# Performance work log

Hardware: AMD Instinct MI355X
Metric: run time of the kernel (lower is better)

The kernel has to match this reference:

```python
import jax, jax.numpy as jnp
import numpy as np

EPS = 1e-5

def setup_inputs() -> dict:
    key = jax.random.key(0)
    k1, k2 = jax.random.split(key)
    N, C, B = 2000000, 32, 16
    data = jax.random.normal(k1, (N, C), dtype=jnp.float32)
    batch_id = jnp.sort(jax.random.randint(k2, (N,), 0, B, dtype=jnp.int32))
    weights = jnp.ones((1, C), dtype=jnp.float32)
    bias = jnp.zeros((1, C), dtype=jnp.float32)
    return {"data": data, "batch_id": batch_id, "batch_size": B,
            "weights": weights, "bias": bias}

def reference(data, batch_id, batch_size, weights, bias):
    # Per-octree (segment) instance norm over nodes, per channel.
    # count[b] = number of nodes in octree b
    ones = jnp.ones((data.shape[0], 1), dtype=data.dtype)
    count = jax.ops.segment_sum(ones, batch_id, num_segments=batch_size)  # [B,1]
    norm = 1.0 / (count + EPS)                                            # [B,1]
    mean = jax.ops.segment_sum(data, batch_id, num_segments=batch_size) * norm  # [B,C]
    out = data - mean[batch_id]                                           # [N,C]
    var = jax.ops.segment_sum(out * out, batch_id, num_segments=batch_size) * norm
    inv_std = 1.0 / jnp.sqrt(var + EPS)                                   # [B,C]
    out = out * inv_std[batch_id]
    return out * weights + bias
```

## Files before the change

kernel.cpp:

```cpp
#include <hip/hip_runtime.h>

#define EPS 1e-5f
#define NB 16
#define NC 32

__global__ __launch_bounds__(256) void oin_stats(
    const float* __restrict__ data,
    const int* __restrict__ batch_id,
    int N, int chunk,
    float* __restrict__ g_sum,
    float* __restrict__ g_sumsq,
    float* __restrict__ g_cnt)
{
    __shared__ float s_sum[NB * NC];
    __shared__ float s_sumsq[NB * NC];
    __shared__ float s_cnt[NB];

    for (int i = threadIdx.x; i < NB * NC; i += 256) { s_sum[i] = 0.f; s_sumsq[i] = 0.f; }
    if (threadIdx.x < NB) s_cnt[threadIdx.x] = 0.f;
    __syncthreads();

    const int c4    = threadIdx.x & 7;
    const int rlane = threadIdx.x >> 3;

    int start = blockIdx.x * chunk;
    int end   = start + chunk;
    if (end > N) end = N;

    const float4* __restrict__ d4 = (const float4*)data;

    float4 a  = make_float4(0.f, 0.f, 0.f, 0.f);
    float4 a2 = make_float4(0.f, 0.f, 0.f, 0.f);
    float  cnt = 0.f;
    int    cur = -1;

    for (int row = start + rlane; row < end; row += 32) {
        int b = batch_id[row];
        if (b != cur) {
            if (cur >= 0) {
                int base = cur * NC + c4 * 4;
                atomicAdd(&s_sum[base + 0], a.x);  atomicAdd(&s_sum[base + 1], a.y);
                atomicAdd(&s_sum[base + 2], a.z);  atomicAdd(&s_sum[base + 3], a.w);
                atomicAdd(&s_sumsq[base + 0], a2.x); atomicAdd(&s_sumsq[base + 1], a2.y);
                atomicAdd(&s_sumsq[base + 2], a2.z); atomicAdd(&s_sumsq[base + 3], a2.w);
                if (c4 == 0) atomicAdd(&s_cnt[cur], cnt);
            }
            cur = b;
            a  = make_float4(0.f, 0.f, 0.f, 0.f);
            a2 = make_float4(0.f, 0.f, 0.f, 0.f);
            cnt = 0.f;
        }
        float4 v = d4[row * 8 + c4];
        a.x  += v.x;       a.y  += v.y;       a.z  += v.z;       a.w  += v.w;
        a2.x += v.x * v.x; a2.y += v.y * v.y; a2.z += v.z * v.z; a2.w += v.w * v.w;
        cnt += 1.f;
    }
    if (cur >= 0) {
        int base = cur * NC + c4 * 4;
        atomicAdd(&s_sum[base + 0], a.x);  atomicAdd(&s_sum[base + 1], a.y);
        atomicAdd(&s_sum[base + 2], a.z);  atomicAdd(&s_sum[base + 3], a.w);
        atomicAdd(&s_sumsq[base + 0], a2.x); atomicAdd(&s_sumsq[base + 1], a2.y);
        atomicAdd(&s_sumsq[base + 2], a2.z); atomicAdd(&s_sumsq[base + 3], a2.w);
        if (c4 == 0) atomicAdd(&s_cnt[cur], cnt);
    }
    __syncthreads();

    for (int i = threadIdx.x; i < NB * NC; i += 256) {
        atomicAdd(&g_sum[i], s_sum[i]);
        atomicAdd(&g_sumsq[i], s_sumsq[i]);
    }
    if (threadIdx.x < NB) atomicAdd(&g_cnt[threadIdx.x], s_cnt[threadIdx.x]);
}

__global__ __launch_bounds__(512) void oin_finalize(
    const float* __restrict__ g_sum, const float* __restrict__ g_sumsq,
    const float* __restrict__ g_cnt,
    const float* __restrict__ weights, const float* __restrict__ bias,
    float* __restrict__ g_scale, float* __restrict__ g_shift)
{
    int tid = threadIdx.x;
    int b = tid >> 5, c = tid & 31;
    float count = g_cnt[b];
    float norm  = 1.f / (count + EPS);
    float mean  = g_sum[tid] * norm;
    float cn    = count * norm;
    float var   = g_sumsq[tid] * norm - (2.f - cn) * mean * mean;
    float inv_std = 1.f / sqrtf(var + EPS);
    float scale = inv_std * weights[c];
    g_scale[tid] = scale;
    g_shift[tid] = bias[c] - mean * scale;
}

__global__ __launch_bounds__(256) void oin_norm(
    const float* __restrict__ data,
    const int* __restrict__ batch_id,
    const float* __restrict__ g_scale,
    const float* __restrict__ g_shift,
    float* __restrict__ out, int n4)
{
    __shared__ float4 s_scale4[NB * NC / 4];
    __shared__ float4 s_shift4[NB * NC / 4];
    {
        float* ss = (float*)s_scale4;
        float* sh = (float*)s_shift4;
        for (int i = threadIdx.x; i < NB * NC; i += 256) {
            ss[i] = g_scale[i];
            sh[i] = g_shift[i];
        }
    }
    __syncthreads();

    const float4* __restrict__ in4 = (const float4*)data;
    float4* __restrict__ out4 = (float4*)out;

    int stride = gridDim.x * 256;
    for (int i = blockIdx.x * 256 + threadIdx.x; i < n4; i += stride) {
        int row = i >> 3;
        int c4  = i & 7;
        int b   = batch_id[row];
        float4 v = in4[i];
        float4 sc = s_scale4[b * 8 + c4];
        float4 sh = s_shift4[b * 8 + c4];
        float4 o;
        o.x = v.x * sc.x + sh.x;
        o.y = v.y * sc.y + sh.y;
        o.z = v.z * sc.z + sh.z;
        o.w = v.w * sc.w + sh.w;
        out4[i] = o;
    }
}

extern "C" void kernel_launch(void* const* d_in, const int* in_sizes, int n_in,
                              void* d_out, int out_size, void* d_ws, size_t ws_size,
                              hipStream_t stream) {
    const float* data     = (const float*)d_in[0];
    const int*   batch_id = (const int*)d_in[1];
    const float* weights  = (const float*)d_in[3];
    const float* bias     = (const float*)d_in[4];
    float* out = (float*)d_out;

    int N = in_sizes[0] / NC;

    float* g_sum   = (float*)d_ws;
    float* g_sumsq = g_sum + NB * NC;
    float* g_cnt   = g_sumsq + NB * NC;
    float* g_scale = g_cnt + NB;
    float* g_shift = g_scale + NB * NC;

    hipMemsetAsync(d_ws, 0, (size_t)(NB * NC * 2 + NB) * sizeof(float), stream);

    const int blocks1 = 1024;
    int chunk = (N + blocks1 - 1) / blocks1;
    oin_stats<<<blocks1, 256, 0, stream>>>(data, batch_id, N, chunk, g_sum, g_sumsq, g_cnt);

    oin_finalize<<<1, 512, 0, stream>>>(g_sum, g_sumsq, g_cnt, weights, bias, g_scale, g_shift);

    int n4 = N * (NC / 4);
    oin_norm<<<2048, 256, 0, stream>>>(data, batch_id, g_scale, g_shift, out, n4);
}
```

Baseline: 526.5 us.

## Add uniform-segment fast paths and fuse finalize into normalize kernel

Stats and normalize kernels now check whether a block's row chunk lies in a single segment. If so, they skip per-row batch_id lookups and use 4-way unrolled float4 loads to expose more memory parallelism. The finalize kernel is removed, and each normalize block recomputes scale/shift from the global sums in shared memory, saving a launch. Global atomics with zero partials are skipped. The cost is a redundant per-block finalize computation and extra code paths.

```diff
diff --git a/kernel.cpp b/kernel.cpp
--- a/kernel.cpp
+++ b/kernel.cpp
@@ -27,16 +27,67 @@
     int end   = start + chunk;
     if (end > N) end = N;
 
-    const float4* __restrict__ d4 = (const float4*)data;
-
-    float4 a  = make_float4(0.f, 0.f, 0.f, 0.f);
-    float4 a2 = make_float4(0.f, 0.f, 0.f, 0.f);
-    float  cnt = 0.f;
-    int    cur = -1;
-
-    for (int row = start + rlane; row < end; row += 32) {
-        int b = batch_id[row];
-        if (b != cur) {
+    if (start < N) {
+        const float4* __restrict__ d4 = (const float4*)data;
+        float4 a  = make_float4(0.f, 0.f, 0.f, 0.f);
+        float4 a2 = make_float4(0.f, 0.f, 0.f, 0.f);
+        float  cnt = 0.f;
+
+        int b0 = batch_id[start];
+        int b1 = batch_id[end - 1];
+
+        if (b0 == b1) {
+            int row = start + rlane;
+            for (; row + 96 < end; row += 128) {
+                float4 v0 = d4[row * 8 + c4];
+                float4 v1 = d4[(row + 32) * 8 + c4];
+                float4 v2 = d4[(row + 64) * 8 + c4];
+                float4 v3 = d4[(row + 96) * 8 + c4];
+                a.x += v0.x; a.y += v0.y; a.z += v0.z; a.w += v0.w;
+                a2.x += v0.x*v0.x; a2.y += v0.y*v0.y; a2.z += v0.z*v0.z; a2.w += v0.w*v0.w;
+                a.x += v1.x; a.y += v1.y; a.z += v1.z; a.w += v1.w;
+                a2.x += v1.x*v1.x; a2.y += v1.y*v1.y; a2.z += v1.z*v1.z; a2.w += v1.w*v1.w;
+                a.x += v2.x; a.y += v2.y; a.z += v2.z; a.w += v2.w;
+                a2.x += v2.x*v2.x; a2.y += v2.y*v2.y; a2.z += v2.z*v2.z; a2.w += v2.w*v2.w;
+                a.x += v3.x; a.y += v3.y; a.z += v3.z; a.w += v3.w;
+                a2.x += v3.x*v3.x; a2.y += v3.y*v3.y; a2.z += v3.z*v3.z; a2.w += v3.w*v3.w;
+                cnt += 4.f;
+            }
+            for (; row < end; row += 32) {
+                float4 v = d4[row * 8 + c4];
+                a.x += v.x; a.y += v.y; a.z += v.z; a.w += v.w;
+                a2.x += v.x*v.x; a2.y += v.y*v.y; a2.z += v.z*v.z; a2.w += v.w*v.w;
+                cnt += 1.f;
+            }
+            int base = b0 * NC + c4 * 4;
+            atomicAdd(&s_sum[base + 0], a.x);  atomicAdd(&s_sum[base + 1], a.y);
+            atomicAdd(&s_sum[base + 2], a.z);  atomicAdd(&s_sum[base + 3], a.w);
+            atomicAdd(&s_sumsq[base + 0], a2.x); atomicAdd(&s_sumsq[base + 1], a2.y);
+            atomicAdd(&s_sumsq[base + 2], a2.z); atomicAdd(&s_sumsq[base + 3], a2.w);
+            if (c4 == 0) atomicAdd(&s_cnt[b0], cnt);
+        } else {
+            int cur = -1;
+            for (int row = start + rlane; row < end; row += 32) {
+                float4 v = d4[row * 8 + c4];
+                int b = batch_id[row];
+                if (b != cur) {
+                    if (cur >= 0) {
+                        int base = cur * NC + c4 * 4;
+                        atomicAdd(&s_sum[base + 0], a.x);  atomicAdd(&s_sum[base + 1], a.y);
+                        atomicAdd(&s_sum[base + 2], a.z);  atomicAdd(&s_sum[base + 3], a.w);
+                        atomicAdd(&s_sumsq[base + 0], a2.x); atomicAdd(&s_sumsq[base + 1], a2.y);
+                        atomicAdd(&s_sumsq[base + 2], a2.z); atomicAdd(&s_sumsq[base + 3], a2.w);
+                        if (c4 == 0) atomicAdd(&s_cnt[cur], cnt);
+                    }
+                    cur = b;
+                    a  = make_float4(0.f, 0.f, 0.f, 0.f);
+                    a2 = make_float4(0.f, 0.f, 0.f, 0.f);
+                    cnt = 0.f;
+                }
+                a.x += v.x; a.y += v.y; a.z += v.z; a.w += v.w;
+                a2.x += v.x*v.x; a2.y += v.y*v.y; a2.z += v.z*v.z; a2.w += v.w*v.w;
+                cnt += 1.f;
+            }
             if (cur >= 0) {
                 int base = cur * NC + c4 * 4;
                 atomicAdd(&s_sum[base + 0], a.x);  atomicAdd(&s_sum[base + 1], a.y);
@@ -45,88 +96,102 @@
                 atomicAdd(&s_sumsq[base + 2], a2.z); atomicAdd(&s_sumsq[base + 3], a2.w);
                 if (c4 == 0) atomicAdd(&s_cnt[cur], cnt);
             }
-            cur = b;
-            a  = make_float4(0.f, 0.f, 0.f, 0.f);
-            a2 = make_float4(0.f, 0.f, 0.f, 0.f);
-            cnt = 0.f;
-        }
-        float4 v = d4[row * 8 + c4];
-        a.x  += v.x;       a.y  += v.y;       a.z  += v.z;       a.w  += v.w;
-        a2.x += v.x * v.x; a2.y += v.y * v.y; a2.z += v.z * v.z; a2.w += v.w * v.w;
-        cnt += 1.f;
-    }
-    if (cur >= 0) {
-        int base = cur * NC + c4 * 4;
-        atomicAdd(&s_sum[base + 0], a.x);  atomicAdd(&s_sum[base + 1], a.y);
-        atomicAdd(&s_sum[base + 2], a.z);  atomicAdd(&s_sum[base + 3], a.w);
-        atomicAdd(&s_sumsq[base + 0], a2.x); atomicAdd(&s_sumsq[base + 1], a2.y);
-        atomicAdd(&s_sumsq[base + 2], a2.z); atomicAdd(&s_sumsq[base + 3], a2.w);
-        if (c4 == 0) atomicAdd(&s_cnt[cur], cnt);
+        }
     }
     __syncthreads();
 
     for (int i = threadIdx.x; i < NB * NC; i += 256) {
-        atomicAdd(&g_sum[i], s_sum[i]);
-        atomicAdd(&g_sumsq[i], s_sumsq[i]);
-    }
-    if (threadIdx.x < NB) atomicAdd(&g_cnt[threadIdx.x], s_cnt[threadIdx.x]);
-}
-
-__global__ __launch_bounds__(512) void oin_finalize(
-    const float* __restrict__ g_sum, const float* __restrict__ g_sumsq,
-    const float* __restrict__ g_cnt,
-    const float* __restrict__ weights, const float* __restrict__ bias,
-    float* __restrict__ g_scale, float* __restrict__ g_shift)
-{
-    int tid = threadIdx.x;
-    int b = tid >> 5, c = tid & 31;
-    float count = g_cnt[b];
-    float norm  = 1.f / (count + EPS);
-    float mean  = g_sum[tid] * norm;
-    float cn    = count * norm;
-    float var   = g_sumsq[tid] * norm - (2.f - cn) * mean * mean;
-    float inv_std = 1.f / sqrtf(var + EPS);
-    float scale = inv_std * weights[c];
-    g_scale[tid] = scale;
-    g_shift[tid] = bias[c] - mean * scale;
+        float s = s_sum[i], q = s_sumsq[i];
+        if (s != 0.f || q != 0.f) {
+            atomicAdd(&g_sum[i], s);
+            atomicAdd(&g_sumsq[i], q);
+        }
+    }
+    if (threadIdx.x < NB) {
+        float c = s_cnt[threadIdx.x];
+        if (c != 0.f) atomicAdd(&g_cnt[threadIdx.x], c);
+    }
 }
 
 __global__ __launch_bounds__(256) void oin_norm(
     const float* __restrict__ data,
     const int* __restrict__ batch_id,
-    const float* __restrict__ g_scale,
-    const float* __restrict__ g_shift,
-    float* __restrict__ out, int n4)
+    const float* __restrict__ g_sum,
+    const float* __restrict__ g_sumsq,
+    const float* __restrict__ g_cnt,
+    const float* __restrict__ weights,
+    const float* __restrict__ bias,
+    float* __restrict__ out, int N, int chunk)
 {
-    __shared__ float4 s_scale4[NB * NC / 4];
-    __shared__ float4 s_shift4[NB * NC / 4];
+    __shared__ float4 s_sc[NB * NC / 4];
+    __shared__ float4 s_sh[NB * NC / 4];
     {
-        float* ss = (float*)s_scale4;
-        float* sh = (float*)s_shift4;
-        for (int i = threadIdx.x; i < NB * NC; i += 256) {
-            ss[i] = g_scale[i];
-            sh[i] = g_shift[i];
+        float* sc = (float*)s_sc;
+        float* sh = (float*)s_sh;
+        for (int t = threadIdx.x; t < NB * NC; t += 256) {
+            int b = t >> 5, c = t & 31;
+            float count = g_cnt[b];
+            float norm  = 1.f / (count + EPS);
+            float mean  = g_sum[t] * norm;
+            float cn    = count * norm;
+            float var   = g_sumsq[t] * norm - (2.f - cn) * mean * mean;
+            float inv_std = 1.f / sqrtf(var + EPS);
+            float scale = inv_std * weights[c];
+            sc[t] = scale;
+            sh[t] = bias[c] - mean * scale;
         }
     }
     __syncthreads();
+
+    int start = blockIdx.x * chunk;
+    int end   = start + chunk;
+    if (end > N) end = N;
+    if (start >= N) return;
 
     const float4* __restrict__ in4 = (const float4*)data;
     float4* __restrict__ out4 = (float4*)out;
 
-    int stride = gridDim.x * 256;
-    for (int i = blockIdx.x * 256 + threadIdx.x; i < n4; i += stride) {
-        int row = i >> 3;
-        int c4  = i & 7;
-        int b   = batch_id[row];
-        float4 v = in4[i];
-        float4 sc = s_scale4[b * 8 + c4];
-        float4 sh = s_shift4[b * 8 + c4];
-        float4 o;
-        o.x = v.x * sc.x + sh.x;
-        o.y = v.y * sc.y + sh.y;
-        o.z = v.z * sc.z + sh.z;
-        o.w = v.w * sc.w + sh.w;
-        out4[i] = o;
+    int e0 = start * 8;
+    int e1 = end * 8;
+
+    int b0 = batch_id[start];
+    int b1 = batch_id[end - 1];
+
+    if (b0 == b1) {
+        float4 sc = s_sc[b0 * 8 + (threadIdx.x & 7)];
+        float4 sh = s_sh[b0 * 8 + (threadIdx.x & 7)];
+        int i = e0 + threadIdx.x;
+        for (; i + 768 < e1; i += 1024) {
+            float4 v0 = in4[i];
+            float4 v1 = in4[i + 256];
+            float4 v2 = in4[i + 512];
+            float4 v3 = in4[i + 768];
+            float4 o0, o1, o2, o3;
+            o0.x = v0.x*sc.x + sh.x; o0.y = v0.y*sc.y + sh.y; o0.z = v0.z*sc.z + sh.z; o0.w = v0.w*sc.w + sh.w;
+            o1.x = v1.x*sc.x + sh.x; o1.y = v1.y*sc.y + sh.y; o1.z = v1.z*sc.z + sh.z; o1.w = v1.w*sc.w + sh.w;
+            o2.x = v2.x*sc.x + sh.x; o2.y = v2.y*sc.y + sh.y; o2.z = v2.z*sc.z + sh.z; o2.w = v2.w*sc.w + sh.w;
+            o3.x = v3.x*sc.x + sh.x; o3.y = v3.y*sc.y + sh.y; o3.z = v3.z*sc.z + sh.z; o3.w = v3.w*sc.w + sh.w;
+            out4[i]       = o0;
+            out4[i + 256] = o1;
+            out4[i + 512] = o2;
+            out4[i + 768] = o3;
+        }
+        for (; i < e1; i += 256) {
+            float4 v = in4[i];
+            float4 o;
+            o.x = v.x*sc.x + sh.x; o.y = v.y*sc.y + sh.y; o.z = v.z*sc.z + sh.z; o.w = v.w*sc.w + sh.w;
+            out4[i] = o;
+        }
+    } else {
+        for (int i = e0 + threadIdx.x; i < e1; i += 256) {
+            float4 v = in4[i];
+            int b = batch_id[i >> 3];
+            float4 sc = s_sc[b * 8 + (i & 7)];
+            float4 sh = s_sh[b * 8 + (i & 7)];
+            float4 o;
+            o.x = v.x*sc.x + sh.x; o.y = v.y*sc.y + sh.y; o.z = v.z*sc.z + sh.z; o.w = v.w*sc.w + sh.w;
+            out4[i] = o;
+        }
     }
 }
 
@@ -144,17 +209,15 @@
     float* g_sum   = (float*)d_ws;
     float* g_sumsq = g_sum + NB * NC;
     float* g_cnt   = g_sumsq + NB * NC;
-    float* g_scale = g_cnt + NB;
-    float* g_shift = g_scale + NB * NC;
 
     hipMemsetAsync(d_ws, 0, (size_t)(NB * NC * 2 + NB) * sizeof(float), stream);
 
     const int blocks1 = 1024;
-    int chunk = (N + blocks1 - 1) / blocks1;
-    oin_stats<<<blocks1, 256, 0, stream>>>(data, batch_id, N, chunk, g_sum, g_sumsq, g_cnt);
-
-    oin_finalize<<<1, 512, 0, stream>>>(g_sum, g_sumsq, g_cnt, weights, bias, g_scale, g_shift);
-
-    int n4 = N * (NC / 4);
-    oin_norm<<<2048, 256, 0, stream>>>(data, batch_id, g_scale, g_shift, out, n4);
+    int chunk1 = (N + blocks1 - 1) / blocks1;
+    oin_stats<<<blocks1, 256, 0, stream>>>(data, batch_id, N, chunk1, g_sum, g_sumsq, g_cnt);
+
+    const int blocks2 = 2048;
+    int chunk2 = (N + blocks2 - 1) / blocks2;
+    oin_norm<<<blocks2, 256, 0, stream>>>(data, batch_id, g_sum, g_sumsq, g_cnt,
+                                          weights, bias, out, N, chunk2);
 }
```

Measured after the change: 501.0 us. 4.8% less time.
